# Kernel tuning notes

Hardware: AMD Instinct MI355X
Metric: run time of the kernel (lower is better)

## Reference

```python
import jax, jax.numpy as jnp
import numpy as np

D_MODEL = 1024
NUM_HEADS = 16
D_K = D_MODEL // NUM_HEADS
THETA = 10000.0
B, S = 2, 2048


def apply_rope(x, token_position, theta=THETA):
    # x: [B, H, S, d_k]; token_position: [B, S] int
    d_k = x.shape[-1]
    inv_freq = 1.0 / theta ** (jnp.arange(0, d_k, 2, dtype=jnp.float32) / d_k)  # [d_k/2]
    angles = token_position.astype(jnp.float32)[:, :, None] * inv_freq[None, None, :]  # [B,S,d_k/2]
    cos = jnp.cos(angles)[:, None, :, :]  # [B,1,S,d_k/2]
    sin = jnp.sin(angles)[:, None, :, :]
    x_even = x[..., 0::2]
    x_odd = x[..., 1::2]
    rot_even = x_even * cos - x_odd * sin
    rot_odd = x_even * sin + x_odd * cos
    # interleave back: stack on new last axis, then flatten
    return jnp.stack([rot_even, rot_odd], axis=-1).reshape(x.shape)


def setup_inputs() -> dict:
    key = jax.random.key(0)
    kx, kq, kk, kv, ko = jax.random.split(key, 5)
    scale = 1.0 / np.sqrt(D_MODEL)
    x = jax.random.normal(kx, (B, S, D_MODEL), dtype=jnp.float32)
    WQ = jax.random.normal(kq, (D_MODEL, D_MODEL), dtype=jnp.float32) * scale
    WK = jax.random.normal(kk, (D_MODEL, D_MODEL), dtype=jnp.float32) * scale
    WV = jax.random.normal(kv, (D_MODEL, D_MODEL), dtype=jnp.float32) * scale
    WO = jax.random.normal(ko, (D_MODEL, D_MODEL), dtype=jnp.float32) * scale
    token_position = jnp.broadcast_to(jnp.arange(S, dtype=jnp.int32)[None, :], (B, S))
    return {"x": x, "token_position": token_position, "WQ": WQ, "WK": WK, "WV": WV, "WO": WO}


def reference(x, token_position, WQ, WK, WV, WO):
    Batch, seq, _ = x.shape
    Q = jnp.einsum('bsd,de->bse', x, WQ).reshape(Batch, seq, NUM_HEADS, D_K).transpose(0, 2, 1, 3)
    K = jnp.einsum('bsd,de->bse', x, WK).reshape(Batch, seq, NUM_HEADS, D_K).transpose(0, 2, 1, 3)
    V = jnp.einsum('bsd,de->bse', x, WV).reshape(Batch, seq, NUM_HEADS, D_K).transpose(0, 2, 1, 3)
    Q = apply_rope(Q, token_position)
    K = apply_rope(K, token_position)
    score = jnp.einsum('bhqd,bhkd->bhqk', Q, K) / jnp.sqrt(jnp.float32(D_K))
    causal = jnp.tril(jnp.ones((seq, seq), dtype=bool))  # [S,S]
    score = jnp.where(causal[None, None, :, :], score, -jnp.inf)
    probs = jax.nn.softmax(score, axis=-1)
    out = jnp.einsum('bhqk,bhkd->bhqd', probs, V)
    out = out.transpose(0, 2, 1, 3).reshape(Batch, seq, D_MODEL)
    return jnp.einsum('bsd,de->bse', out, WO)
```

## Files before the change

kernel.cpp:

```cpp
#include <hip/hip_runtime.h>
#include <hip/hip_bf16.h>

typedef __attribute__((ext_vector_type(8))) short short8;
typedef __attribute__((ext_vector_type(4))) float f32x4;
typedef __hip_bfloat16 bf16_t;

#define SEQ 2048
#define DM 1024
#define NH 16
#define DK 64

static __device__ __forceinline__ f32x4 mfma16x16x32(short8 a, short8 b, f32x4 c) {
  return __builtin_amdgcn_mfma_f32_16x16x32_bf16(a, b, c, 0, 0, 0);
}

__global__ void sniff_dtype(const unsigned int* __restrict__ x, int* __restrict__ flag) {
  int lane = threadIdx.x & 63;
  int cnt = 0;
  for (int r = 0; r < 4; ++r) {
    unsigned int v = x[lane + r * 64];
    int e = (v >> 7) & 0xFF;
    if (e >= 100 && e <= 145) cnt++;
  }
  for (int d = 1; d < 64; d <<= 1) cnt += __shfl_xor(cnt, d, 64);
  if (lane == 0) *flag = (cnt >= 192) ? 1 : 0;
}

__global__ __launch_bounds__(256) void prep(const void* __restrict__ x,
                                            bf16_t* __restrict__ Xc,
                                            const void* __restrict__ w0,
                                            const void* __restrict__ w1,
                                            const void* __restrict__ w2,
                                            const void* __restrict__ w3,
                                            bf16_t* __restrict__ wt_base,
                                            const int* __restrict__ tokpos,
                                            float2* __restrict__ rtab,
                                            const int* __restrict__ flag) {
  int f = *flag;
  int bx = blockIdx.x, t = threadIdx.x;
  __shared__ bf16_t tile[64][65];
  if (bx < 4096) {
    int i = bx * 256 + t;
    if (f) {
      ((uint2*)Xc)[i] = ((const uint2*)x)[i];
    } else {
      const float4 v = ((const float4*)x)[i];
      bf16_t o[4] = {__float2bfloat16(v.x), __float2bfloat16(v.y),
                     __float2bfloat16(v.z), __float2bfloat16(v.w)};
      ((uint2*)Xc)[i] = *(const uint2*)o;
    }
  } else if (bx < 5120) {
    int rem = bx - 4096;
    int z = rem >> 8, bxx = rem & 15, byy = (rem >> 4) & 15;
    const void* src = (z == 0) ? w0 : (z == 1) ? w1 : (z == 2) ? w2 : w3;
    bf16_t* dst = wt_base + (size_t)((z + 1) & 3) * DM * DM;
    int tx = t & 63, ty = t >> 6;
    int r0 = byy * 64, c0 = bxx * 64;
    for (int i = 0; i < 64; i += 4) {
      size_t idx = (size_t)(r0 + ty + i) * DM + c0 + tx;
      tile[ty + i][tx] = f ? ((const bf16_t*)src)[idx]
                           : __float2bfloat16(((const float*)src)[idx]);
    }
    __syncthreads();
    for (int i = 0; i < 64; i += 4)
      dst[(size_t)(c0 + ty + i) * DM + r0 + tx] = tile[tx][ty + i];
  } else {
    int i = (bx - 5120) * 256 + t;
    int m = i >> 5, pp = i & 31;
    float pos = (float)tokpos[m];
    float invf = __powf(10000.0f, -(float)pp * (1.0f / 32.0f));
    float sn, cs;
    sincosf(pos * invf, &sn, &cs);
    rtab[i] = make_float2(cs, sn);
  }
}

__global__ __launch_bounds__(256) void gemm128_qkv(const bf16_t* __restrict__ A,
                                                   const bf16_t* __restrict__ WTqkv,
                                                   bf16_t* __restrict__ Qb,
                                                   bf16_t* __restrict__ Kb,
                                                   bf16_t* __restrict__ VTo,
                                                   const float2* __restrict__ rtab) {
  __shared__ __align__(16) char smem[36864];
  bf16_t (*As)[72] = (bf16_t(*)[72])smem;
  bf16_t (*Bs)[72] = (bf16_t(*)[72])(smem + 18432);
  int t = threadIdx.x;
  int w = t >> 6, lane = t & 63, l15 = lane & 15, quad = lane >> 4;
  int wrow = w >> 1, wcol = w & 1;
  int m0 = blockIdx.y * 128, nx = blockIdx.x, n0 = nx * 128;
  int srow = t >> 1, scol = (t & 1) * 32;
  const bf16_t* ag = A + (size_t)(m0 + srow) * DM + scol;
  const bf16_t* bg = WTqkv + (size_t)(n0 + srow) * DM + scol;
  f32x4 acc[4][4] = {};
  for (int kk = 0; kk < DM; kk += 64) {
    short8 a0 = *(const short8*)(ag + kk);
    short8 a1 = *(const short8*)(ag + kk + 8);
    short8 a2 = *(const short8*)(ag + kk + 16);
    short8 a3 = *(const short8*)(ag + kk + 24);
    short8 b0 = *(const short8*)(bg + kk);
    short8 b1 = *(const short8*)(bg + kk + 8);
    short8 b2 = *(const short8*)(bg + kk + 16);
    short8 b3 = *(const short8*)(bg + kk + 24);
    __syncthreads();
    *(short8*)&As[srow][scol] = a0;       *(short8*)&As[srow][scol + 8] = a1;
    *(short8*)&As[srow][scol + 16] = a2;  *(short8*)&As[srow][scol + 24] = a3;
    *(short8*)&Bs[srow][scol] = b0;       *(short8*)&Bs[srow][scol + 8] = b1;
    *(short8*)&Bs[srow][scol + 16] = b2;  *(short8*)&Bs[srow][scol + 24] = b3;
    __syncthreads();
    short8 af[4][2], bfr[4][2];
#pragma unroll
    for (int mt = 0; mt < 4; ++mt) {
      af[mt][0] = *(const short8*)&As[wrow * 64 + mt * 16 + l15][quad * 8];
      af[mt][1] = *(const short8*)&As[wrow * 64 + mt * 16 + l15][32 + quad * 8];
    }
#pragma unroll
    for (int nt = 0; nt < 4; ++nt) {
      bfr[nt][0] = *(const short8*)&Bs[wcol * 64 + nt * 16 + l15][quad * 8];
      bfr[nt][1] = *(const short8*)&Bs[wcol * 64 + nt * 16 + l15][32 + quad * 8];
    }
#pragma unroll
    for (int mt = 0; mt < 4; ++mt)
#pragma unroll
      for (int nt = 0; nt < 4; ++nt) {
        acc[mt][nt] = mfma16x16x32(af[mt][0], bfr[nt][0], acc[mt][nt]);
        acc[mt][nt] = mfma16x16x32(af[mt][1], bfr[nt][1], acc[mt][nt]);
      }
  }

  int sel = nx >> 3;
  int nc = (nx & 7) * 128;
  __syncthreads();
  bf16_t (*Tw)[72] = (bf16_t(*)[72])(smem + w * 9216);
  int b = m0 >> 11;
  int h = (nc >> 6) + wcol;
  if (sel < 2) {
    bf16_t* dst = sel ? Kb : Qb;
    float sgnv = (l15 & 1) ? 1.0f : -1.0f;
#pragma unroll
    for (int mt = 0; mt < 4; ++mt)
#pragma unroll
      for (int r = 0; r < 4; ++r) {
        int m = m0 + wrow * 64 + mt * 16 + quad * 4 + r;
        const float2* tr = rtab + m * 32;
#pragma unroll
        for (int nt = 0; nt < 4; ++nt) {
          int d = nt * 16 + l15;
          float val = acc[mt][nt][r];
          float partner = __shfl_xor(val, 1, 64);
          float2 cssn = tr[d >> 1];
          Tw[mt * 16 + quad * 4 + r][d] = __float2bfloat16(val * cssn.x + sgnv * partner * cssn.y);
        }
      }
    int s_base = (m0 & (SEQ - 1)) + wrow * 64;
    bf16_t* dq = dst + ((size_t)(b * NH + h) * SEQ + s_base) * DK;
#pragma unroll
    for (int c = 0; c < 8; ++c) {
      int row = c * 8 + (lane >> 3);
      int col = (lane & 7) * 8;
      *(short8*)&dq[(size_t)row * DK + col] = *(const short8*)&Tw[row][col];
    }
  } else {
#pragma unroll
    for (int mt = 0; mt < 4; ++mt)
#pragma unroll
      for (int nt = 0; nt < 4; ++nt)
#pragma unroll
        for (int r = 0; r < 4; ++r)
          Tw[nt * 16 + l15][mt * 16 + quad * 4 + r] = __float2bfloat16(acc[mt][nt][r]);
    int s_base = m0 & (SEQ - 1);
#pragma unroll
    for (int c = 0; c < 4; ++c) {
      int d = c * 16 + (lane >> 2);
      int s2 = (lane & 3) * 16;
      size_t ob = ((size_t)(b * NH + h) * DK + d) * SEQ + s_base + wrow * 64 + s2;
      *(short8*)&VTo[ob] = *(const short8*)&Tw[d][s2];
      *(short8*)&VTo[ob + 8] = *(const short8*)&Tw[d][s2 + 8];
    }
  }
}

__global__ __launch_bounds__(256) void gemm128_out(const bf16_t* __restrict__ A,
                                                   const bf16_t* __restrict__ BT,
                                                   void* __restrict__ out,
                                                   const int* __restrict__ flag) {
  __shared__ __align__(16) bf16_t As[128][72];
  __shared__ __align__(16) bf16_t Bs[128][72];
  int f = *flag;
  int t = threadIdx.x;
  int w = t >> 6, lane = t & 63, l15 = lane & 15, quad = lane >> 4;
  int wrow = w >> 1, wcol = w & 1;
  int m0 = blockIdx.y * 128, n0 = blockIdx.x * 128;
  int srow = t >> 1, scol = (t & 1) * 32;
  const bf16_t* ag = A + (size_t)(m0 + srow) * DM + scol;
  const bf16_t* bg = BT + (size_t)(n0 + srow) * DM + scol;
  f32x4 acc[4][4] = {};
  for (int kk = 0; kk < DM; kk += 64) {
    short8 a0 = *(const short8*)(ag + kk);
    short8 a1 = *(const short8*)(ag + kk + 8);
    short8 a2 = *(const short8*)(ag + kk + 16);
    short8 a3 = *(const short8*)(ag + kk + 24);
    short8 b0 = *(const short8*)(bg + kk);
    short8 b1 = *(const short8*)(bg + kk + 8);
    short8 b2 = *(const short8*)(bg + kk + 16);
    short8 b3 = *(const short8*)(bg + kk + 24);
    __syncthreads();
    *(short8*)&As[srow][scol] = a0;       *(short8*)&As[srow][scol + 8] = a1;
    *(short8*)&As[srow][scol + 16] = a2;  *(short8*)&As[srow][scol + 24] = a3;
    *(short8*)&Bs[srow][scol] = b0;       *(short8*)&Bs[srow][scol + 8] = b1;
    *(short8*)&Bs[srow][scol + 16] = b2;  *(short8*)&Bs[srow][scol + 24] = b3;
    __syncthreads();
    short8 af[4][2], bfr[4][2];
#pragma unroll
    for (int mt = 0; mt < 4; ++mt) {
      af[mt][0] = *(const short8*)&As[wrow * 64 + mt * 16 + l15][quad * 8];
      af[mt][1] = *(const short8*)&As[wrow * 64 + mt * 16 + l15][32 + quad * 8];
    }
#pragma unroll
    for (int nt = 0; nt < 4; ++nt) {
      bfr[nt][0] = *(const short8*)&Bs[wcol * 64 + nt * 16 + l15][quad * 8];
      bfr[nt][1] = *(const short8*)&Bs[wcol * 64 + nt * 16 + l15][32 + quad * 8];
    }
#pragma unroll
    for (int mt = 0; mt < 4; ++mt)
#pragma unroll
      for (int nt = 0; nt < 4; ++nt) {
        acc[mt][nt] = mfma16x16x32(af[mt][0], bfr[nt][0], acc[mt][nt]);
        acc[mt][nt] = mfma16x16x32(af[mt][1], bfr[nt][1], acc[mt][nt]);
      }
  }
#pragma unroll
  for (int mt = 0; mt < 4; ++mt)
#pragma unroll
    for (int nt = 0; nt < 4; ++nt)
#pragma unroll
      for (int r = 0; r < 4; ++r) {
        int m = m0 + wrow * 64 + mt * 16 + quad * 4 + r;
        int col = n0 + wcol * 64 + nt * 16 + l15;
        size_t oidx = (size_t)m * DM + col;
        if (f) ((bf16_t*)out)[oidx] = __float2bfloat16(acc[mt][nt][r]);
        else   ((float*)out)[oidx] = acc[mt][nt][r];
      }
}

__global__ __launch_bounds__(256) void attn_fwd(const bf16_t* __restrict__ Q,
                                                const bf16_t* __restrict__ K,
                                                const bf16_t* __restrict__ VT,
                                                bf16_t* __restrict__ O) {
  int x = blockIdx.x, bh = blockIdx.y;
  int b = bh >> 4, h = bh & 15;
  int g = x + (bh << 4);
  int raw = (g + (g >> 8)) & 15;
  const int pmap[16] = {0, 15, 1, 13, 2, 12, 3, 11, 4, 10, 5, 9, 6, 8, 7, 14};
  int p = pmap[raw];
  int qA = p, qB = 31 - p;
  int t = threadIdx.x;
  int w = t >> 6, lane = t & 63, l15 = lane & 15, quad = lane >> 4;
  const size_t base = (size_t)bh * SEQ * DK;
  const bf16_t* Qp = Q + base;
  const bf16_t* Kp = K + base;
  const bf16_t* VTp = VT + base;

  __shared__ __align__(16) bf16_t Ks[64][72];
  __shared__ __align__(16) bf16_t Vs[64][72];
  __shared__ __align__(16) bf16_t Pb[4][2][16][72];

  int rowA = qA * 64 + w * 16 + l15;
  int rowB = qB * 64 + w * 16 + l15;
  short8 qfA0 = *(const short8*)(Qp + (size_t)rowA * DK + quad * 8);
  short8 qfA1 = *(const short8*)(Qp + (size_t)rowA * DK + 32 + quad * 8);
  short8 qfB0 = *(const short8*)(Qp + (size_t)rowB * DK + quad * 8);
  short8 qfB1 = *(const short8*)(Qp + (size_t)rowB * DK + 32 + quad * 8);

  int srow = t >> 2, scoff = (t & 3) * 16;
  const bf16_t* kst = Kp + (size_t)srow * DK + scoff;
  const bf16_t* vst = VTp + (size_t)srow * SEQ + scoff;

  short8 kA = *(const short8*)(kst);
  short8 kB = *(const short8*)(kst + 8);
  short8 vA = *(const short8*)(vst);
  short8 vB = *(const short8*)(vst + 8);

  f32x4 oA[4] = {}, oB[4] = {};
  float rA[4] = {0.f, 0.f, 0.f, 0.f}, rB[4] = {0.f, 0.f, 0.f, 0.f};

  for (int kb = 0; kb <= qB; ++kb) {
    __syncthreads();
    *(short8*)&Ks[srow][scoff] = kA;
    *(short8*)&Ks[srow][scoff + 8] = kB;
    *(short8*)&Vs[srow][scoff] = vA;
    *(short8*)&Vs[srow][scoff + 8] = vB;
    __syncthreads();

    int nkb = (kb < qB) ? (kb + 1) : qB;
    kA = *(const short8*)(kst + (size_t)nkb * 64 * DK);
    kB = *(const short8*)(kst + (size_t)nkb * 64 * DK + 8);
    vA = *(const short8*)(vst + (size_t)nkb * 64);
    vB = *(const short8*)(vst + (size_t)nkb * 64 + 8);

    bool doA = (kb <= qA);

    {
      f32x4 sc[4];
#pragma unroll
      for (int kt = 0; kt < 4; ++kt) {
        f32x4 a = {};
        a = mfma16x16x32(qfB0, *(const short8*)&Ks[kt * 16 + l15][quad * 8], a);
        a = mfma16x16x32(qfB1, *(const short8*)&Ks[kt * 16 + l15][32 + quad * 8], a);
        sc[kt] = a;
      }
      bool diag = (kb == qB);
#pragma unroll
      for (int kt = 0; kt < 4; ++kt)
#pragma unroll
        for (int reg = 0; reg < 4; ++reg) {
          float sv = sc[kt][reg] * 0.125f;
          if (diag) {
            int kg = kt * 16 + l15, qg = w * 16 + quad * 4 + reg;
            if (kg > qg) sv = -30000.0f;
          }
          float pp = __expf(sv);
          rB[reg] += pp;
          Pb[w][1][quad * 4 + reg][kt * 16 + l15] = __float2bfloat16(pp);
        }
      short8 p0 = *(const short8*)&Pb[w][1][l15][quad * 8];
      short8 p1 = *(const short8*)&Pb[w][1][l15][32 + quad * 8];
#pragma unroll
      for (int dt = 0; dt < 4; ++dt) {
        oB[dt] = mfma16x16x32(p0, *(const short8*)&Vs[dt * 16 + l15][quad * 8], oB[dt]);
        oB[dt] = mfma16x16x32(p1, *(const short8*)&Vs[dt * 16 + l15][32 + quad * 8], oB[dt]);
      }
    }
    if (doA) {
      f32x4 sc[4];
#pragma unroll
      for (int kt = 0; kt < 4; ++kt) {
        f32x4 a = {};
        a = mfma16x16x32(qfA0, *(const short8*)&Ks[kt * 16 + l15][quad * 8], a);
        a = mfma16x16x32(qfA1, *(const short8*)&Ks[kt * 16 + l15][32 + quad * 8], a);
        sc[kt] = a;
      }
      bool diag = (kb == qA);
#pragma unroll
      for (int kt = 0; kt < 4; ++kt)
#pragma unroll
        for (int reg = 0; reg < 4; ++reg) {
          float sv = sc[kt][reg] * 0.125f;
          if (diag) {
            int kg = kt * 16 + l15, qg = w * 16 + quad * 4 + reg;
            if (kg > qg) sv = -30000.0f;
          }
          float pp = __expf(sv);
          rA[reg] += pp;
          Pb[w][0][quad * 4 + reg][kt * 16 + l15] = __float2bfloat16(pp);
        }
      short8 p0 = *(const short8*)&Pb[w][0][l15][quad * 8];
      short8 p1 = *(const short8*)&Pb[w][0][l15][32 + quad * 8];
#pragma unroll
      for (int dt = 0; dt < 4; ++dt) {
        oA[dt] = mfma16x16x32(p0, *(const short8*)&Vs[dt * 16 + l15][quad * 8], oA[dt]);
        oA[dt] = mfma16x16x32(p1, *(const short8*)&Vs[dt * 16 + l15][32 + quad * 8], oA[dt]);
      }
    }
  }

  for (int d = 1; d < 16; d <<= 1)
#pragma unroll
    for (int reg = 0; reg < 4; ++reg) {
      rA[reg] += __shfl_xor(rA[reg], d, 64);
      rB[reg] += __shfl_xor(rB[reg], d, 64);
    }

#pragma unroll
  for (int dt = 0; dt < 4; ++dt)
#pragma unroll
    for (int reg = 0; reg < 4; ++reg) {
      int col = h * DK + dt * 16 + l15;
      int qa = qA * 64 + w * 16 + quad * 4 + reg;
      int qb_ = qB * 64 + w * 16 + quad * 4 + reg;
      O[((size_t)b * SEQ + qa) * DM + col] = __float2bfloat16(oA[dt][reg] / rA[reg]);
      O[((size_t)b * SEQ + qb_) * DM + col] = __float2bfloat16(oB[dt][reg] / rB[reg]);
    }
}

extern "C" void kernel_launch(void* const* d_in, const int* in_sizes, int n_in,
                              void* d_out, int out_size, void* d_ws, size_t ws_size,
                              hipStream_t stream) {
  const void* x = d_in[0];
  const int* tokpos = (const int*)d_in[1];
  const void* WQ = d_in[2];
  const void* WK = d_in[3];
  const void* WV = d_in[4];
  const void* WO = d_in[5];

  char* ws = (char*)d_ws;
  const size_t MB = 1024 * 1024;
  bf16_t* WT  = (bf16_t*)ws;
  bf16_t* Xc  = (bf16_t*)(ws + 8 * MB);
  bf16_t* Qb  = (bf16_t*)(ws + 16 * MB);
  bf16_t* Kb  = (bf16_t*)(ws + 24 * MB);
  bf16_t* VTb = (bf16_t*)(ws + 32 * MB);
  bf16_t* Ab  = (bf16_t*)(ws + 8 * MB);
  int* flag   = (int*)(ws + 40 * MB);
  float2* rtab = (float2*)(ws + 41 * MB);

  dim3 blk(256);
  sniff_dtype<<<1, 64, 0, stream>>>((const unsigned int*)x, flag);
  prep<<<5632, blk, 0, stream>>>(x, Xc, WQ, WK, WV, WO, WT, tokpos, rtab, flag);
  gemm128_qkv<<<dim3(24, 32), blk, 0, stream>>>(Xc, WT + (size_t)DM * DM, Qb, Kb, VTb, rtab);
  attn_fwd<<<dim3(16, 32), blk, 0, stream>>>(Qb, Kb, VTb, Ab);
  gemm128_out<<<dim3(8, 32), blk, 0, stream>>>(Ab, WT, d_out, flag);
}
```

Before: 206.1 us.

## Triple-buffer GEMM tiles via async global-to-LDS loads with XOR swizzle

Both projection GEMMs (QKV and output) now fill a three-stage LDS ring with `global_load_lds` direct copies. The next-but-one K tile is prefetched while the current one is consumed, using explicit `vmcnt` waits and a single barrier per iteration. LDS rows are unpadded and use an XOR swizzle on 16-byte column groups to avoid bank conflicts. This is meant to hide global load latency and drop the register round-trip and the second barrier. In exchange it needs 96KB of dynamic LDS per block, which lowers occupancy, and it relies on inline-asm wait counts being correct.

```diff
diff --git a/kernel.cpp b/kernel.cpp
--- a/kernel.cpp
+++ b/kernel.cpp
@@ -9,9 +9,28 @@
 #define DM 1024
 #define NH 16
 #define DK 64
+#define NKT 16
 
 static __device__ __forceinline__ f32x4 mfma16x16x32(short8 a, short8 b, f32x4 c) {
   return __builtin_amdgcn_mfma_f32_16x16x32_bf16(a, b, c, 0, 0, 0);
+}
+
+typedef const __attribute__((address_space(1))) unsigned int ga_u32_t;
+typedef __attribute__((address_space(3))) unsigned int lds_u32_t;
+static __device__ __forceinline__ void gld16(const bf16_t* g, bf16_t* l) {
+  __builtin_amdgcn_global_load_lds((ga_u32_t*)g, (lds_u32_t*)l, 16, 0, 0);
+}
+static __device__ __forceinline__ void bar() { asm volatile("s_barrier" ::: "memory"); }
+static __device__ __forceinline__ void wait_vm8() { asm volatile("s_waitcnt vmcnt(8)" ::: "memory"); }
+static __device__ __forceinline__ void wait_vm0() { asm volatile("s_waitcnt vmcnt(0)" ::: "memory"); }
+
+static __device__ __forceinline__ void stage_tile(const bf16_t* asrc, const bf16_t* bsrc,
+                                                  char* bufbase, int w, int kk) {
+#pragma unroll
+  for (int j = 0; j < 4; ++j) {
+    gld16(asrc + (size_t)(j * 32) * DM + kk, (bf16_t*)(bufbase + j * 4096 + w * 1024));
+    gld16(bsrc + (size_t)(j * 32) * DM + kk, (bf16_t*)(bufbase + 16384 + j * 4096 + w * 1024));
+  }
 }
 
 __global__ void sniff_dtype(const unsigned int* __restrict__ x, int* __restrict__ flag) {
@@ -81,42 +100,38 @@
                                                    bf16_t* __restrict__ Kb,
                                                    bf16_t* __restrict__ VTo,
                                                    const float2* __restrict__ rtab) {
-  __shared__ __align__(16) char smem[36864];
-  bf16_t (*As)[72] = (bf16_t(*)[72])smem;
-  bf16_t (*Bs)[72] = (bf16_t(*)[72])(smem + 18432);
+  extern __shared__ char smem[];
   int t = threadIdx.x;
   int w = t >> 6, lane = t & 63, l15 = lane & 15, quad = lane >> 4;
   int wrow = w >> 1, wcol = w & 1;
   int m0 = blockIdx.y * 128, nx = blockIdx.x, n0 = nx * 128;
-  int srow = t >> 1, scol = (t & 1) * 32;
-  const bf16_t* ag = A + (size_t)(m0 + srow) * DM + scol;
-  const bf16_t* bg = WTqkv + (size_t)(n0 + srow) * DM + scol;
+  int srow0 = w * 8 + (lane >> 3);
+  int scg = (lane & 7) ^ (lane >> 3);
+  const bf16_t* asrc = A + (size_t)(m0 + srow0) * DM + scg * 8;
+  const bf16_t* bsrc = WTqkv + (size_t)(n0 + srow0) * DM + scg * 8;
+
   f32x4 acc[4][4] = {};
-  for (int kk = 0; kk < DM; kk += 64) {
-    short8 a0 = *(const short8*)(ag + kk);
-    short8 a1 = *(const short8*)(ag + kk + 8);
-    short8 a2 = *(const short8*)(ag + kk + 16);
-    short8 a3 = *(const short8*)(ag + kk + 24);
-    short8 b0 = *(const short8*)(bg + kk);
-    short8 b1 = *(const short8*)(bg + kk + 8);
-    short8 b2 = *(const short8*)(bg + kk + 16);
-    short8 b3 = *(const short8*)(bg + kk + 24);
-    __syncthreads();
-    *(short8*)&As[srow][scol] = a0;       *(short8*)&As[srow][scol + 8] = a1;
-    *(short8*)&As[srow][scol + 16] = a2;  *(short8*)&As[srow][scol + 24] = a3;
-    *(short8*)&Bs[srow][scol] = b0;       *(short8*)&Bs[srow][scol + 8] = b1;
-    *(short8*)&Bs[srow][scol + 16] = b2;  *(short8*)&Bs[srow][scol + 24] = b3;
-    __syncthreads();
+  stage_tile(asrc, bsrc, smem, w, 0);
+  stage_tile(asrc, bsrc, smem + 32768, w, 64);
+  for (int kt = 0; kt < NKT; ++kt) {
+    if (kt < NKT - 1) wait_vm8(); else wait_vm0();
+    bar();
+    if (kt + 2 < NKT)
+      stage_tile(asrc, bsrc, smem + ((kt + 2) % 3) * 32768, w, (kt + 2) * 64);
+    const bf16_t* Ab = (const bf16_t*)(smem + (kt % 3) * 32768);
+    const bf16_t* Bb = Ab + 8192;
     short8 af[4][2], bfr[4][2];
 #pragma unroll
     for (int mt = 0; mt < 4; ++mt) {
-      af[mt][0] = *(const short8*)&As[wrow * 64 + mt * 16 + l15][quad * 8];
-      af[mt][1] = *(const short8*)&As[wrow * 64 + mt * 16 + l15][32 + quad * 8];
+      int r = wrow * 64 + mt * 16 + l15;
+      af[mt][0] = *(const short8*)(Ab + r * 64 + ((quad ^ (l15 & 7)) * 8));
+      af[mt][1] = *(const short8*)(Ab + r * 64 + (((4 + quad) ^ (l15 & 7)) * 8));
     }
 #pragma unroll
     for (int nt = 0; nt < 4; ++nt) {
-      bfr[nt][0] = *(const short8*)&Bs[wcol * 64 + nt * 16 + l15][quad * 8];
-      bfr[nt][1] = *(const short8*)&Bs[wcol * 64 + nt * 16 + l15][32 + quad * 8];
+      int r = wcol * 64 + nt * 16 + l15;
+      bfr[nt][0] = *(const short8*)(Bb + r * 64 + ((quad ^ (l15 & 7)) * 8));
+      bfr[nt][1] = *(const short8*)(Bb + r * 64 + (((4 + quad) ^ (l15 & 7)) * 8));
     }
 #pragma unroll
     for (int mt = 0; mt < 4; ++mt)
@@ -183,42 +198,39 @@
                                                    const bf16_t* __restrict__ BT,
                                                    void* __restrict__ out,
                                                    const int* __restrict__ flag) {
-  __shared__ __align__(16) bf16_t As[128][72];
-  __shared__ __align__(16) bf16_t Bs[128][72];
+  extern __shared__ char smem[];
   int f = *flag;
   int t = threadIdx.x;
   int w = t >> 6, lane = t & 63, l15 = lane & 15, quad = lane >> 4;
   int wrow = w >> 1, wcol = w & 1;
   int m0 = blockIdx.y * 128, n0 = blockIdx.x * 128;
-  int srow = t >> 1, scol = (t & 1) * 32;
-  const bf16_t* ag = A + (size_t)(m0 + srow) * DM + scol;
-  const bf16_t* bg = BT + (size_t)(n0 + srow) * DM + scol;
+  int srow0 = w * 8 + (lane >> 3);
+  int scg = (lane & 7) ^ (lane >> 3);
+  const bf16_t* asrc = A + (size_t)(m0 + srow0) * DM + scg * 8;
+  const bf16_t* bsrc = BT + (size_t)(n0 + srow0) * DM + scg * 8;
+
   f32x4 acc[4][4] = {};
-  for (int kk = 0; kk < DM; kk += 64) {
-    short8 a0 = *(const short8*)(ag + kk);
-    short8 a1 = *(const short8*)(ag + kk + 8);
-    short8 a2 = *(const short8*)(ag + kk + 16);
-    short8 a3 = *(const short8*)(ag + kk + 24);
-    short8 b0 = *(const short8*)(bg + kk);
-    short8 b1 = *(const short8*)(bg + kk + 8);
-    short8 b2 = *(const short8*)(bg + kk + 16);
-    short8 b3 = *(const short8*)(bg + kk + 24);
-    __syncthreads();
-    *(short8*)&As[srow][scol] = a0;       *(short8*)&As[srow][scol + 8] = a1;
-    *(short8*)&As[srow][scol + 16] = a2;  *(short8*)&As[srow][scol + 24] = a3;
-    *(short8*)&Bs[srow][scol] = b0;       *(short8*)&Bs[srow][scol + 8] = b1;
-    *(short8*)&Bs[srow][scol + 16] = b2;  *(short8*)&Bs[srow][scol + 24] = b3;
-    __syncthreads();
+  stage_tile(asrc, bsrc, smem, w, 0);
+  stage_tile(asrc, bsrc, smem + 32768, w, 64);
+  for (int kt = 0; kt < NKT; ++kt) {
+    if (kt < NKT - 1) wait_vm8(); else wait_vm0();
+    bar();
+    if (kt + 2 < NKT)
+      stage_tile(asrc, bsrc, smem + ((kt + 2) % 3) * 32768, w, (kt + 2) * 64);
+    const bf16_t* Ab = (const bf16_t*)(smem + (kt % 3) * 32768);
+    const bf16_t* Bb = Ab + 8192;
     short8 af[4][2], bfr[4][2];
 #pragma unroll
     for (int mt = 0; mt < 4; ++mt) {
-      af[mt][0] = *(const short8*)&As[wrow * 64 + mt * 16 + l15][quad * 8];
-      af[mt][1] = *(const short8*)&As[wrow * 64 + mt * 16 + l15][32 + quad * 8];
+      int r = wrow * 64 + mt * 16 + l15;
+      af[mt][0] = *(const short8*)(Ab + r * 64 + ((quad ^ (l15 & 7)) * 8));
+      af[mt][1] = *(const short8*)(Ab + r * 64 + (((4 + quad) ^ (l15 & 7)) * 8));
     }
 #pragma unroll
     for (int nt = 0; nt < 4; ++nt) {
-      bfr[nt][0] = *(const short8*)&Bs[wcol * 64 + nt * 16 + l15][quad * 8];
-      bfr[nt][1] = *(const short8*)&Bs[wcol * 64 + nt * 16 + l15][32 + quad * 8];
+      int r = wcol * 64 + nt * 16 + l15;
+      bfr[nt][0] = *(const short8*)(Bb + r * 64 + ((quad ^ (l15 & 7)) * 8));
+      bfr[nt][1] = *(const short8*)(Bb + r * 64 + (((4 + quad) ^ (l15 & 7)) * 8));
     }
 #pragma unroll
     for (int mt = 0; mt < 4; ++mt)
@@ -404,9 +416,10 @@
   float2* rtab = (float2*)(ws + 41 * MB);
 
   dim3 blk(256);
+  const size_t gemm_lds = 3 * 32768;
   sniff_dtype<<<1, 64, 0, stream>>>((const unsigned int*)x, flag);
   prep<<<5632, blk, 0, stream>>>(x, Xc, WQ, WK, WV, WO, WT, tokpos, rtab, flag);
-  gemm128_qkv<<<dim3(24, 32), blk, 0, stream>>>(Xc, WT + (size_t)DM * DM, Qb, Kb, VTb, rtab);
+  gemm128_qkv<<<dim3(24, 32), blk, gemm_lds, stream>>>(Xc, WT + (size_t)DM * DM, Qb, Kb, VTb, rtab);
   attn_fwd<<<dim3(16, 32), blk, 0, stream>>>(Qb, Kb, VTb, Ab);
-  gemm128_out<<<dim3(8, 32), blk, 0, stream>>>(Ab, WT, d_out, flag);
-}
+  gemm128_out<<<dim3(8, 32), blk, gemm_lds, stream>>>(Ab, WT, d_out, flag);
+}
```

New measurement: 196.5 us. 1.05x faster.
